# Optimization experiments

Measured on AMD Instinct MI355X. Metric: run time of the kernel, lower is better.

Reference implementation:

```python
import jax, jax.numpy as jnp
import numpy as np
import math

N = 4_194_304
EPS = 1e-07
CENTER_WEIGHT = 2.0
SIZE_WEIGHT = 1.0


def _make_boxes(kxy, kwh):
    # valid xyxy boxes: top-left in [0,600), width/height in [1,41)
    xy = jax.random.uniform(kxy, (N, 2), dtype=jnp.float32) * 600.0
    wh = jax.random.uniform(kwh, (N, 2), dtype=jnp.float32) * 40.0 + 1.0
    return jnp.concatenate([xy, xy + wh], axis=1)


def setup_inputs() -> dict:
    key = jax.random.key(0)
    k1, k2, k3, k4 = jax.random.split(key, 4)
    return {
        "pred_boxes": _make_boxes(k1, k2),
        "target_boxes": _make_boxes(k3, k4),
    }


def reference(pred_boxes, target_boxes):
    # Only the diagonal of the NxN pairwise CIoU tensors is used by the
    # original module, so compute the matched-pair terms directly (same math).
    px1, py1, px2, py2 = (pred_boxes[:, i] for i in range(4))
    tx1, ty1, tx2, ty2 = (target_boxes[:, i] for i in range(4))

    inter_w = jnp.clip(jnp.minimum(px2, tx2) - jnp.maximum(px1, tx1), 0.0)
    inter_h = jnp.clip(jnp.minimum(py2, ty2) - jnp.maximum(py1, ty1), 0.0)
    inter = inter_w * inter_h
    p_area = (px2 - px1) * (py2 - py1)
    t_area = (tx2 - tx1) * (ty2 - ty1)
    iou = inter / (p_area + t_area - inter + EPS)

    pcx, pcy = (px1 + px2) * 0.5, (py1 + py2) * 0.5
    tcx, tcy = (tx1 + tx2) * 0.5, (ty1 + ty2) * 0.5
    center_dist_sq = (pcx - tcx) ** 2 + (pcy - tcy) ** 2

    c_w = jnp.maximum(px2, tx2) - jnp.minimum(px1, tx1)
    c_h = jnp.maximum(py2, ty2) - jnp.minimum(py1, ty1)
    c_diag_sq = c_w ** 2 + c_h ** 2 + EPS  # bbox_iou adds eps here

    iou_term = 1.0 - iou
    # forward() adds eps again on top of c_diag_sq's eps (faithful to source)
    center_term = center_dist_sq / (c_diag_sq + EPS)

    pw, ph = px2 - px1, py2 - py1
    tw, th = tx2 - tx1, ty2 - ty1
    size_term = ((pw - tw) / (tw + EPS)) ** 2 + ((ph - th) / (th + EPS)) ** 2

    loss = iou_term + CENTER_WEIGHT * center_term + SIZE_WEIGHT * size_term
    return jnp.mean(loss)
```

## Files before the change

kernel.cpp:

```cpp
#include <hip/hip_runtime.h>


#define EPSF 1e-7f
#define UNROLL 4
#define BLOCK 256
#define TILE (BLOCK * UNROLL)

__device__ __forceinline__ float fast_rcp(float x) {
    return __builtin_amdgcn_rcpf(x);
}

__device__ __forceinline__ float ciou_elem(float4 p, float4 t) {
    const float px1 = p.x, py1 = p.y, px2 = p.z, py2 = p.w;
    const float tx1 = t.x, ty1 = t.y, tx2 = t.z, ty2 = t.w;

    float iw = fminf(px2, tx2) - fmaxf(px1, tx1);
    float ih = fminf(py2, ty2) - fmaxf(py1, ty1);
    iw = fmaxf(iw, 0.f);
    ih = fmaxf(ih, 0.f);
    const float inter  = iw * ih;
    const float pw = px2 - px1, ph = py2 - py1;
    const float tw = tx2 - tx1, th = ty2 - ty1;
    const float p_area = pw * ph;
    const float t_area = tw * th;
    const float iou = inter * fast_rcp(p_area + t_area - inter + EPSF);

    const float dcx = 0.5f * ((px1 + px2) - (tx1 + tx2));
    const float dcy = 0.5f * ((py1 + py2) - (ty1 + ty2));
    const float center_dist_sq = dcx * dcx + dcy * dcy;
    const float cw = fmaxf(px2, tx2) - fminf(px1, tx1);
    const float ch = fmaxf(py2, ty2) - fminf(py1, ty1);
    const float c_diag_sq = cw * cw + ch * ch + EPSF;
    const float center_term = center_dist_sq * fast_rcp(c_diag_sq + EPSF);

    const float sw = (pw - tw) * fast_rcp(tw + EPSF);
    const float sh = (ph - th) * fast_rcp(th + EPSF);
    const float size_term = sw * sw + sh * sh;

    return (1.f - iou) + 2.f * center_term + size_term;
}

__device__ __forceinline__ float wave_block_reduce(float acc, float* lds_ws) {
    #pragma unroll
    for (int off = 32; off > 0; off >>= 1)
        acc += __shfl_down(acc, off, 64);
    const int lane = threadIdx.x & 63;
    const int wave = threadIdx.x >> 6;
    if (lane == 0) lds_ws[wave] = acc;
    __syncthreads();
    float s = 0.f;
    if (threadIdx.x == 0) {
        #pragma unroll
        for (int w = 0; w < BLOCK / 64; ++w) s += lds_ws[w];
    }
    return s;
}

template <bool TAIL>
__global__ __launch_bounds__(BLOCK) void ciou_partial_kernel(
        const float4* __restrict__ pred,
        const float4* __restrict__ targ,
        float* __restrict__ partial, int n) {
    const int base = blockIdx.x * TILE + threadIdx.x;

    float4 p[UNROLL], t[UNROLL];
    #pragma unroll
    for (int u = 0; u < UNROLL; ++u) {
        int idx = base + u * BLOCK;
        if (TAIL) idx = idx < n ? idx : 0;
        p[u] = pred[idx];
        t[u] = targ[idx];
    }
    __builtin_amdgcn_sched_barrier(0);

    float acc0 = 0.f, acc1 = 0.f;
    #pragma unroll
    for (int u = 0; u < UNROLL; u += 2) {
        if (!TAIL || (base + u * BLOCK) < n)       acc0 += ciou_elem(p[u], t[u]);
        if (!TAIL || (base + (u + 1) * BLOCK) < n) acc1 += ciou_elem(p[u + 1], t[u + 1]);
    }
    float acc = acc0 + acc1;

    __shared__ float lds_ws[BLOCK / 64];
    const float blk = wave_block_reduce(acc, lds_ws);
    if (threadIdx.x == 0) partial[blockIdx.x] = blk;
}

__global__ __launch_bounds__(BLOCK) void ciou_final_kernel(
        const float* __restrict__ partial, int nparts,
        float* __restrict__ out, float inv_n) {
    const float4* pv = (const float4*)partial;
    const int nvec = nparts >> 2;
    float acc = 0.f;
    for (int i = threadIdx.x; i < nvec; i += BLOCK) {
        const float4 v = pv[i];
        acc += (v.x + v.y) + (v.z + v.w);
    }
    __shared__ float lds_ws[BLOCK / 64];
    const float s = wave_block_reduce(acc, lds_ws);
    if (threadIdx.x == 0) out[0] = s * inv_n;
}

extern "C" void kernel_launch(void* const* d_in, const int* in_sizes, int n_in,
                              void* d_out, int out_size, void* d_ws, size_t ws_size,
                              hipStream_t stream) {
    const float4* pred = (const float4*)d_in[0];
    const float4* targ = (const float4*)d_in[1];
    float* out = (float*)d_out;
    float* partial = (float*)d_ws;

    const int n = in_sizes[0] / 4;
    const int grid = (n + TILE - 1) / TILE;

    if (n % TILE == 0) {
        ciou_partial_kernel<false><<<grid, BLOCK, 0, stream>>>(pred, targ, partial, n);
    } else {
        ciou_partial_kernel<true><<<grid, BLOCK, 0, stream>>>(pred, targ, partial, n);
    }
    ciou_final_kernel<<<1, BLOCK, 0, stream>>>(partial, grid, out, 1.0f / (float)n);
}
```

Baseline: 27.77 us.

## Fuse final reduction via atomicAdd and use inline-asm SGPR-based vector loads

Replaces the two-kernel partial-sum plus final-reduce scheme with a single kernel in which each block atomically adds its scaled partial sum into the output, zeroed by a memset beforehand. The main path issues global_load_dwordx4 through inline assembly with a scalar base and 32-bit vector offsets, followed by an explicit waitcnt. This removes the second kernel launch and the workspace round trip, and shrinks address arithmetic. In exchange it adds a memset, 4096 atomics on one address, and a summation order that is no longer deterministic.

After: 67.21 us. 2.42x slower.

```diff
diff --git a/kernel.cpp b/kernel.cpp
--- a/kernel.cpp
+++ b/kernel.cpp
@@ -8,6 +8,15 @@
 
 __device__ __forceinline__ float fast_rcp(float x) {
     return __builtin_amdgcn_rcpf(x);
+}
+
+__device__ __forceinline__ float4 gload4(unsigned long long sbase, unsigned voff) {
+    float4 r;
+    asm volatile("global_load_dwordx4 %0, %1, %2"
+                 : "=v"(r)
+                 : "v"(voff), "s"(sbase)
+                 : "memory");
+    return r;
 }
 
 __device__ __forceinline__ float ciou_elem(float4 p, float4 t) {
@@ -40,65 +49,56 @@
     return (1.f - iou) + 2.f * center_term + size_term;
 }
 
-__device__ __forceinline__ float wave_block_reduce(float acc, float* lds_ws) {
+template <bool TAIL>
+__global__ __launch_bounds__(BLOCK) void ciou_fused_kernel(
+        const float4* __restrict__ pred,
+        const float4* __restrict__ targ,
+        float* __restrict__ out, int n, float inv_n) {
+    float acc0 = 0.f, acc1 = 0.f;
+
+    if (!TAIL) {
+        const unsigned base = (blockIdx.x * TILE + threadIdx.x) * 16u;
+        float4 p[UNROLL], t[UNROLL];
+        #pragma unroll
+        for (int u = 0; u < UNROLL; ++u) {
+            const unsigned off = base + (unsigned)(u * BLOCK * 16);
+            p[u] = gload4((unsigned long long)pred, off);
+            t[u] = gload4((unsigned long long)targ, off);
+        }
+        asm volatile("s_waitcnt vmcnt(0)" ::: "memory");
+        __builtin_amdgcn_sched_barrier(0);
+
+        #pragma unroll
+        for (int u = 0; u < UNROLL; u += 2) {
+            acc0 += ciou_elem(p[u],     t[u]);
+            acc1 += ciou_elem(p[u + 1], t[u + 1]);
+        }
+    } else {
+        const int base = blockIdx.x * TILE + threadIdx.x;
+        #pragma unroll
+        for (int u = 0; u < UNROLL; ++u) {
+            const int idx = base + u * BLOCK;
+            if (idx < n) acc0 += ciou_elem(pred[idx], targ[idx]);
+        }
+    }
+    float acc = acc0 + acc1;
+
     #pragma unroll
     for (int off = 32; off > 0; off >>= 1)
         acc += __shfl_down(acc, off, 64);
+
+    __shared__ float lds_ws[BLOCK / 64];
     const int lane = threadIdx.x & 63;
     const int wave = threadIdx.x >> 6;
     if (lane == 0) lds_ws[wave] = acc;
     __syncthreads();
-    float s = 0.f;
+
     if (threadIdx.x == 0) {
+        float blk = 0.f;
         #pragma unroll
-        for (int w = 0; w < BLOCK / 64; ++w) s += lds_ws[w];
+        for (int w = 0; w < BLOCK / 64; ++w) blk += lds_ws[w];
+        atomicAdd(out, blk * inv_n);
     }
-    return s;
-}
-
-template <bool TAIL>
-__global__ __launch_bounds__(BLOCK) void ciou_partial_kernel(
-        const float4* __restrict__ pred,
-        const float4* __restrict__ targ,
-        float* __restrict__ partial, int n) {
-    const int base = blockIdx.x * TILE + threadIdx.x;
-
-    float4 p[UNROLL], t[UNROLL];
-    #pragma unroll
-    for (int u = 0; u < UNROLL; ++u) {
-        int idx = base + u * BLOCK;
-        if (TAIL) idx = idx < n ? idx : 0;
-        p[u] = pred[idx];
-        t[u] = targ[idx];
-    }
-    __builtin_amdgcn_sched_barrier(0);
-
-    float acc0 = 0.f, acc1 = 0.f;
-    #pragma unroll
-    for (int u = 0; u < UNROLL; u += 2) {
-        if (!TAIL || (base + u * BLOCK) < n)       acc0 += ciou_elem(p[u], t[u]);
-        if (!TAIL || (base + (u + 1) * BLOCK) < n) acc1 += ciou_elem(p[u + 1], t[u + 1]);
-    }
-    float acc = acc0 + acc1;
-
-    __shared__ float lds_ws[BLOCK / 64];
-    const float blk = wave_block_reduce(acc, lds_ws);
-    if (threadIdx.x == 0) partial[blockIdx.x] = blk;
-}
-
-__global__ __launch_bounds__(BLOCK) void ciou_final_kernel(
-        const float* __restrict__ partial, int nparts,
-        float* __restrict__ out, float inv_n) {
-    const float4* pv = (const float4*)partial;
-    const int nvec = nparts >> 2;
-    float acc = 0.f;
-    for (int i = threadIdx.x; i < nvec; i += BLOCK) {
-        const float4 v = pv[i];
-        acc += (v.x + v.y) + (v.z + v.w);
-    }
-    __shared__ float lds_ws[BLOCK / 64];
-    const float s = wave_block_reduce(acc, lds_ws);
-    if (threadIdx.x == 0) out[0] = s * inv_n;
 }
 
 extern "C" void kernel_launch(void* const* d_in, const int* in_sizes, int n_in,
@@ -107,15 +107,16 @@
     const float4* pred = (const float4*)d_in[0];
     const float4* targ = (const float4*)d_in[1];
     float* out = (float*)d_out;
-    float* partial = (float*)d_ws;
 
     const int n = in_sizes[0] / 4;
     const int grid = (n + TILE - 1) / TILE;
+    const float inv_n = 1.0f / (float)n;
+
+    hipMemsetAsync(d_out, 0, sizeof(float), stream);
 
     if (n % TILE == 0) {
-        ciou_partial_kernel<false><<<grid, BLOCK, 0, stream>>>(pred, targ, partial, n);
+        ciou_fused_kernel<false><<<grid, BLOCK, 0, stream>>>(pred, targ, out, n, inv_n);
     } else {
-        ciou_partial_kernel<true><<<grid, BLOCK, 0, stream>>>(pred, targ, partial, n);
+        ciou_fused_kernel<true><<<grid, BLOCK, 0, stream>>>(pred, targ, out, n, inv_n);
     }
-    ciou_final_kernel<<<1, BLOCK, 0, stream>>>(partial, grid, out, 1.0f / (float)n);
 }
```

## Use persistent fixed grid with double-buffered software-pipelined loads

Applied to the files above, without the earlier changes.

Replaces the one-tile-per-block launch (4096 blocks of 1024 elements) with a fixed grid of 2048 blocks. Each block walks its own contiguous chunk in stages of 512 elements, with two register buffers so the next stage's loads are issued before the current stage is computed. The aim is to keep more memory requests in flight per thread, overlap compute with loads, and cut block launch and reduction overhead. It also halves the number of partial sums for the final kernel. The cost is higher register use, and a grid-stride fallback kernel is used when the size does not divide evenly.

New measurement: 27.50 us. No clear change (-1.0%).

```diff
diff --git a/kernel.cpp b/kernel.cpp
--- a/kernel.cpp
+++ b/kernel.cpp
@@ -2,9 +2,10 @@
 
 
 #define EPSF 1e-7f
-#define UNROLL 4
 #define BLOCK 256
-#define TILE (BLOCK * UNROLL)
+#define U 2
+#define STAGE_ELEMS (BLOCK * U)
+#define GRID 2048
 
 __device__ __forceinline__ float fast_rcp(float x) {
     return __builtin_amdgcn_rcpf(x);
@@ -56,31 +57,60 @@
     return s;
 }
 
-template <bool TAIL>
-__global__ __launch_bounds__(BLOCK) void ciou_partial_kernel(
+__global__ __launch_bounds__(BLOCK) void ciou_partial_pipe(
+        const float4* __restrict__ pred,
+        const float4* __restrict__ targ,
+        float* __restrict__ partial, int nstages) {
+    const long long blockBase =
+        (long long)blockIdx.x * nstages * STAGE_ELEMS + threadIdx.x;
+    const float4* pb = pred + blockBase;
+    const float4* tb = targ + blockBase;
+
+    float4 pA[U], tA[U], pB[U], tB[U];
+
+#define LOAD(PX, TX, s)                                   \
+    _Pragma("unroll")                                     \
+    for (int u = 0; u < U; ++u) {                         \
+        PX[u] = pb[(s) * STAGE_ELEMS + u * BLOCK];        \
+        TX[u] = tb[(s) * STAGE_ELEMS + u * BLOCK];        \
+    }
+
+    float acc0 = 0.f, acc1 = 0.f;
+#define COMPUTE(PX, TX)                                   \
+    acc0 += ciou_elem(PX[0], TX[0]);                      \
+    acc1 += ciou_elem(PX[1], TX[1]);
+
+    LOAD(pA, tA, 0)
+    LOAD(pB, tB, 1)
+
+    int s = 2;
+    for (; s < nstages; s += 2) {
+        COMPUTE(pA, tA)
+        LOAD(pA, tA, s)
+        COMPUTE(pB, tB)
+        LOAD(pB, tB, s + 1)
+    }
+    COMPUTE(pA, tA)
+    COMPUTE(pB, tB)
+
+#undef LOAD
+#undef COMPUTE
+
+    float acc = acc0 + acc1;
+    __shared__ float lds_ws[BLOCK / 64];
+    const float blk = wave_block_reduce(acc, lds_ws);
+    if (threadIdx.x == 0) partial[blockIdx.x] = blk;
+}
+
+__global__ __launch_bounds__(BLOCK) void ciou_partial_generic(
         const float4* __restrict__ pred,
         const float4* __restrict__ targ,
         float* __restrict__ partial, int n) {
-    const int base = blockIdx.x * TILE + threadIdx.x;
-
-    float4 p[UNROLL], t[UNROLL];
-    #pragma unroll
-    for (int u = 0; u < UNROLL; ++u) {
-        int idx = base + u * BLOCK;
-        if (TAIL) idx = idx < n ? idx : 0;
-        p[u] = pred[idx];
-        t[u] = targ[idx];
-    }
-    __builtin_amdgcn_sched_barrier(0);
-
-    float acc0 = 0.f, acc1 = 0.f;
-    #pragma unroll
-    for (int u = 0; u < UNROLL; u += 2) {
-        if (!TAIL || (base + u * BLOCK) < n)       acc0 += ciou_elem(p[u], t[u]);
-        if (!TAIL || (base + (u + 1) * BLOCK) < n) acc1 += ciou_elem(p[u + 1], t[u + 1]);
-    }
-    float acc = acc0 + acc1;
-
+    const int tid = blockIdx.x * BLOCK + threadIdx.x;
+    const int stride = GRID * BLOCK;
+    float acc = 0.f;
+    for (int i = tid; i < n; i += stride)
+        acc += ciou_elem(pred[i], targ[i]);
     __shared__ float lds_ws[BLOCK / 64];
     const float blk = wave_block_reduce(acc, lds_ws);
     if (threadIdx.x == 0) partial[blockIdx.x] = blk;
@@ -110,12 +140,14 @@
     float* partial = (float*)d_ws;
 
     const int n = in_sizes[0] / 4;
-    const int grid = (n + TILE - 1) / TILE;
+    const int per_block_stage = STAGE_ELEMS;
+    const long long denom = (long long)GRID * per_block_stage;
+    const int nstages = (int)(n / denom);
 
-    if (n % TILE == 0) {
-        ciou_partial_kernel<false><<<grid, BLOCK, 0, stream>>>(pred, targ, partial, n);
+    if ((long long)nstages * denom == n && nstages >= 2 && (nstages & 1) == 0) {
+        ciou_partial_pipe<<<GRID, BLOCK, 0, stream>>>(pred, targ, partial, nstages);
     } else {
-        ciou_partial_kernel<true><<<grid, BLOCK, 0, stream>>>(pred, targ, partial, n);
+        ciou_partial_generic<<<GRID, BLOCK, 0, stream>>>(pred, targ, partial, n);
     }
-    ciou_final_kernel<<<1, BLOCK, 0, stream>>>(partial, grid, out, 1.0f / (float)n);
+    ciou_final_kernel<<<1, BLOCK, 0, stream>>>(partial, GRID, out, 1.0f / (float)n);
 }
```
